# Optimization experiments

Measured on AMD Instinct MI355X. Metric: run time of the kernel, lower is better.

The kernel has to match this reference:

```python
import jax, jax.numpy as jnp
import numpy as np
import math

H_DIM = 1024
N_HEADS = 16
B, T = 2, 2048


def setup_inputs() -> dict:
    key = jax.random.key(0)
    ks = jax.random.split(key, 9)
    scale = 1.0 / math.sqrt(H_DIM)
    x = jax.random.normal(ks[0], (B, T, H_DIM), dtype=jnp.float32)
    Wq = jax.random.normal(ks[1], (H_DIM, H_DIM), dtype=jnp.float32) * scale
    Wk = jax.random.normal(ks[2], (H_DIM, H_DIM), dtype=jnp.float32) * scale
    Wv = jax.random.normal(ks[3], (H_DIM, H_DIM), dtype=jnp.float32) * scale
    Wp = jax.random.normal(ks[4], (H_DIM, H_DIM), dtype=jnp.float32) * scale
    bq = jnp.zeros((H_DIM,), dtype=jnp.float32)
    bk = jnp.zeros((H_DIM,), dtype=jnp.float32)
    bv = jnp.zeros((H_DIM,), dtype=jnp.float32)
    bp = jnp.zeros((H_DIM,), dtype=jnp.float32)
    return {"x": x, "Wq": Wq, "bq": bq, "Wk": Wk, "bk": bk,
            "Wv": Wv, "bv": bv, "Wp": Wp, "bp": bp}


def _attention(x, Wq, bq, Wk, bk, Wv, bv, Wp, bp):
    Bx, Tx, C = x.shape
    N = N_HEADS
    D = C // N
    # torch Linear: x @ W.T + b
    q = (x @ Wq.T + bq).reshape(Bx, Tx, N, D).transpose(0, 2, 1, 3)  # [B,N,T,D]
    k = (x @ Wk.T + bk).reshape(Bx, Tx, N, D).transpose(0, 2, 1, 3)
    v = (x @ Wv.T + bv).reshape(Bx, Tx, N, D).transpose(0, 2, 1, 3)
    scores = jnp.einsum('bntd,bnsd->bnts', q, k) / math.sqrt(D)  # [B,N,T,T]
    causal = jnp.tril(jnp.ones((Tx, Tx), dtype=bool))
    scores = jnp.where(causal[None, None], scores, -jnp.inf)
    probs = jax.nn.softmax(scores, axis=-1)
    attn = jnp.einsum('bnts,bnsd->bntd', probs, v)  # [B,N,T,D]
    attn = attn.transpose(0, 2, 1, 3).reshape(Bx, Tx, C)
    return attn @ Wp.T + bp


def reference(x, Wq, bq, Wk, bk, Wv, bv, Wp, bp):
    return _attention(x, Wq, bq, Wk, bk, Wv, bv, Wp, bp)
```

## Files before the change

### kernel.cpp

```cpp
#include <hip/hip_runtime.h>
#include <hip/hip_bf16.h>
#include <math.h>

#define TSEQ 2048
#define CDIM 1024
#define NHEADS 16
#define DHEAD 64
#define BSZ 2
#define MROWS (BSZ * TSEQ)
#define SCALE_Q 0.18033688f

typedef __attribute__((ext_vector_type(8))) short short8;
typedef __attribute__((ext_vector_type(4))) short short4v;
typedef __attribute__((ext_vector_type(4))) float f32x4;

__device__ inline f32x4 mfma16(short8 a, short8 b, f32x4 c) {
    return __builtin_amdgcn_mfma_f32_16x16x32_bf16(a, b, c, 0, 0, 0);
}

__device__ inline short f2bf(float f) {
    __hip_bfloat16 h = __float2bfloat16(f);
    return __builtin_bit_cast(short, h);
}

__global__ __launch_bounds__(256) void convx_kernel(const float* __restrict__ x,
                                                    short* __restrict__ xb) {
    size_t off = (size_t)(blockIdx.x * 256 + threadIdx.x) * 8;
    float4 a = *(const float4*)(x + off);
    float4 b = *(const float4*)(x + off + 4);
    short8 h;
    h[0] = f2bf(a.x); h[1] = f2bf(a.y); h[2] = f2bf(a.z); h[3] = f2bf(a.w);
    h[4] = f2bf(b.x); h[5] = f2bf(b.y); h[6] = f2bf(b.z); h[7] = f2bf(b.w);
    *(short8*)(xb + off) = h;
}

__global__ __launch_bounds__(256, 3) void gemm_qkv(
    const short* __restrict__ xb, const float* __restrict__ Wq,
    const float* __restrict__ Wk, const float* __restrict__ Wv,
    const float* __restrict__ bq, const float* __restrict__ bk,
    const float* __restrict__ bv, short* __restrict__ qws,
    short* __restrict__ kws, short* __restrict__ vtws) {
    __shared__ __attribute__((aligned(16))) short a_lds[128][72];
    __shared__ __attribute__((aligned(16))) short b_lds[128][72];

    const int tid = threadIdx.x;
    const int lane = tid & 63;
    const int wv = tid >> 6;
    const int wr = wv >> 1, wc = wv & 1;
    const int l15 = lane & 15, l4 = lane >> 4;
    const int mbase = blockIdx.x * 128;
    const int which = blockIdx.y >> 3;
    const int nbase = (blockIdx.y & 7) * 128;
    const float* Wf = which == 0 ? Wq : (which == 1 ? Wk : Wv);
    const float* bias = which == 0 ? bq : (which == 1 ? bk : bv);

    f32x4 acc[4][4];
#pragma unroll
    for (int i = 0; i < 4; ++i)
#pragma unroll
        for (int j = 0; j < 4; ++j) acc[i][j] = f32x4{0.f, 0.f, 0.f, 0.f};

    const int ar = tid >> 3;
    const int ag = (tid & 7) * 8;
    const int br = tid >> 4;
    const int bg = (tid & 15) * 4;
    const short* aptr = xb + (size_t)(mbase + ar) * CDIM + ag;
    const float* bptr = Wf + (size_t)(nbase + br) * CDIM + bg;

    short8 apre[4];
    float4 bpre[8];
#pragma unroll
    for (int it = 0; it < 4; ++it)
        apre[it] = *(const short8*)(aptr + (size_t)(32 * it) * CDIM);
#pragma unroll
    for (int it = 0; it < 8; ++it)
        bpre[it] = *(const float4*)(bptr + (size_t)(16 * it) * CDIM);

    for (int k0 = 0; k0 < CDIM; k0 += 64) {
        __syncthreads();
#pragma unroll
        for (int it = 0; it < 4; ++it)
            *(short8*)&a_lds[ar + 32 * it][ag] = apre[it];
#pragma unroll
        for (int it = 0; it < 8; ++it) {
            short4v h;
            h.x = f2bf(bpre[it].x); h.y = f2bf(bpre[it].y);
            h.z = f2bf(bpre[it].z); h.w = f2bf(bpre[it].w);
            *(short4v*)&b_lds[br + 16 * it][bg] = h;
        }
        __syncthreads();
        if (k0 + 64 < CDIM) {
#pragma unroll
            for (int it = 0; it < 4; ++it)
                apre[it] = *(const short8*)(aptr + (size_t)(32 * it) * CDIM + k0 + 64);
#pragma unroll
            for (int it = 0; it < 8; ++it)
                bpre[it] = *(const float4*)(bptr + (size_t)(16 * it) * CDIM + k0 + 64);
        }

#pragma unroll
        for (int kk = 0; kk < 2; ++kk) {
            short8 af[4], bfr[4];
#pragma unroll
            for (int i = 0; i < 4; ++i)
                af[i] = *(const short8*)&a_lds[wr * 64 + i * 16 + l15][kk * 32 + l4 * 8];
#pragma unroll
            for (int j = 0; j < 4; ++j)
                bfr[j] = *(const short8*)&b_lds[wc * 64 + j * 16 + l15][kk * 32 + l4 * 8];
#pragma unroll
            for (int i = 0; i < 4; ++i)
#pragma unroll
                for (int j = 0; j < 4; ++j)
                    acc[i][j] = mfma16(af[i], bfr[j], acc[i][j]);
        }
    }

    if (which < 2) {
        short* dst = which == 0 ? qws : kws;
        const float scale = which == 0 ? SCALE_Q : 1.0f;
#pragma unroll
        for (int i = 0; i < 4; ++i) {
            int mrow = mbase + wr * 64 + i * 16 + l4 * 4;
#pragma unroll
            for (int j = 0; j < 4; ++j) {
                int o = nbase + wc * 64 + j * 16 + l15;
                int n = o >> 6, d = o & 63;
                float bval = bias[o];
#pragma unroll
                for (int r = 0; r < 4; ++r) {
                    int mm = mrow + r;
                    int bb = mm >> 11;
                    int t = mm & (TSEQ - 1);
                    dst[(((size_t)bb * NHEADS + n) * TSEQ + t) * DHEAD + d] =
                        f2bf((acc[i][j][r] + bval) * scale);
                }
            }
        }
    } else {
#pragma unroll
        for (int i = 0; i < 4; ++i) {
            int mrow = mbase + wr * 64 + i * 16 + l4 * 4;
            int bb = mrow >> 11;
            int t = mrow & (TSEQ - 1);
#pragma unroll
            for (int j = 0; j < 4; ++j) {
                int o = nbase + wc * 64 + j * 16 + l15;
                int n = o >> 6, d = o & 63;
                float bval = bias[o];
                short4v h4;
#pragma unroll
                for (int r = 0; r < 4; ++r) h4[r] = f2bf(acc[i][j][r] + bval);
                *(short4v*)&vtws[(((size_t)bb * NHEADS + n) * DHEAD + d) * TSEQ + t] = h4;
            }
        }
    }
}

__global__ __launch_bounds__(256) void gemm_p(
    const short* __restrict__ attn, const short* __restrict__ wpb,
    const float* __restrict__ bp, float* __restrict__ out) {
    __shared__ __attribute__((aligned(16))) short a_lds[64][40];
    __shared__ __attribute__((aligned(16))) short b_lds[128][40];

    const int tid = threadIdx.x;
    const int lane = tid & 63;
    const int wv = tid >> 6;
    const int wr = wv >> 1, wc = wv & 1;
    const int l15 = lane & 15, l4 = lane >> 4;
    const int mbase = blockIdx.x * 64;
    const int nbase = blockIdx.y * 128;

    f32x4 acc[2][4];
#pragma unroll
    for (int i = 0; i < 2; ++i)
#pragma unroll
        for (int j = 0; j < 4; ++j) acc[i][j] = f32x4{0.f, 0.f, 0.f, 0.f};

    const int arow = tid >> 2;
    const int acol = (tid & 3) * 8;
    const short* aptr = attn + (size_t)(mbase + arow) * CDIM + acol;
    const short* bptr = wpb + (size_t)(nbase + arow) * CDIM + acol;

    short8 apre, bpre[2];
    apre = *(const short8*)(aptr);
    bpre[0] = *(const short8*)(bptr);
    bpre[1] = *(const short8*)(bptr + (size_t)64 * CDIM);

    for (int k0 = 0; k0 < CDIM; k0 += 32) {
        __syncthreads();
        *(short8*)&a_lds[arow][acol] = apre;
        *(short8*)&b_lds[arow][acol] = bpre[0];
        *(short8*)&b_lds[arow + 64][acol] = bpre[1];
        __syncthreads();
        if (k0 + 32 < CDIM) {
            apre = *(const short8*)(aptr + k0 + 32);
            bpre[0] = *(const short8*)(bptr + k0 + 32);
            bpre[1] = *(const short8*)(bptr + (size_t)64 * CDIM + k0 + 32);
        }

        short8 af[2], bfr[4];
#pragma unroll
        for (int i = 0; i < 2; ++i)
            af[i] = *(const short8*)&a_lds[wr * 32 + i * 16 + l15][l4 * 8];
#pragma unroll
        for (int j = 0; j < 4; ++j)
            bfr[j] = *(const short8*)&b_lds[wc * 64 + j * 16 + l15][l4 * 8];
#pragma unroll
        for (int i = 0; i < 2; ++i)
#pragma unroll
            for (int j = 0; j < 4; ++j)
                acc[i][j] = mfma16(af[i], bfr[j], acc[i][j]);
    }

#pragma unroll
    for (int i = 0; i < 2; ++i) {
        int mrow = mbase + wr * 32 + i * 16 + l4 * 4;
#pragma unroll
        for (int j = 0; j < 4; ++j) {
            int o = nbase + wc * 64 + j * 16 + l15;
            float bval = bp[o];
#pragma unroll
            for (int r = 0; r < 4; ++r)
                out[(size_t)(mrow + r) * CDIM + o] = acc[i][j][r] + bval;
        }
    }
}

__global__ __launch_bounds__(256) void attn_kernel(
    const short* __restrict__ q, const short* __restrict__ k,
    const short* __restrict__ vt, short* __restrict__ attn_out) {
    __shared__ __attribute__((aligned(16))) short k_lds[128][64];
    __shared__ __attribute__((aligned(16))) short vt_lds[64][128];
    __shared__ __attribute__((aligned(16))) short p_lds[4][16][136];

    const int tid = threadIdx.x;
    const int w = tid >> 6;
    const int lane = tid & 63;
    const int l15 = lane & 15;
    const int l4 = lane >> 4;
    const int h = blockIdx.x;
    const int qtile = gridDim.y - 1 - blockIdx.y;
    const int wrow0 = qtile * 64 + w * 16;

    short8 qf[2];
#pragma unroll
    for (int kh = 0; kh < 2; ++kh)
        qf[kh] = *(const short8*)(q + ((size_t)h * TSEQ + wrow0 + l15) * DHEAD +
                                  kh * 32 + l4 * 8);

    float l_run[4];
    f32x4 o_acc[4];
#pragma unroll
    for (int r = 0; r < 4; ++r) l_run[r] = 0.f;
#pragma unroll
    for (int dt = 0; dt < 4; ++dt) o_acc[dt] = f32x4{0.f, 0.f, 0.f, 0.f};

    const int ntiles = (qtile + 2) >> 1;
    const size_t kbase = (size_t)h * TSEQ * DHEAD;
    const size_t vbase = (size_t)h * DHEAD * TSEQ;

    const int ksrow = tid >> 3, ksg = tid & 7;
    const int vsrow = tid >> 4, vsg = tid & 15;

    short8 kpre[4], vpre[4];
#pragma unroll
    for (int it = 0; it < 4; ++it) {
        kpre[it] = *(const short8*)(k + kbase + (size_t)(ksrow + it * 32) * DHEAD + ksg * 8);
        vpre[it] = *(const short8*)(vt + vbase + (size_t)(vsrow + it * 16) * TSEQ + vsg * 8);
    }

    for (int kvt = 0; kvt < ntiles; ++kvt) {
        const int kvbase = kvt * 128;
        __syncthreads();
#pragma unroll
        for (int it = 0; it < 4; ++it) {
            int krow = ksrow + it * 32;
            *(short8*)&k_lds[krow][(ksg ^ (krow & 7)) * 8] = kpre[it];
            int vrow = vsrow + it * 16;
            *(short8*)&vt_lds[vrow][((vsg ^ (vrow & 15))) * 8] = vpre[it];
        }
        __syncthreads();
        if (kvt + 1 < ntiles) {
            int kvb2 = kvbase + 128;
#pragma unroll
            for (int it = 0; it < 4; ++it) {
                kpre[it] = *(const short8*)(k + kbase + (size_t)(kvb2 + ksrow + it * 32) * DHEAD + ksg * 8);
                vpre[it] = *(const short8*)(vt + vbase + (size_t)(vsrow + it * 16) * TSEQ + kvb2 + vsg * 8);
            }
        }

        f32x4 s[8];
#pragma unroll
        for (int jt = 0; jt < 8; ++jt) {
            int row = jt * 16 + l15;
            int sw = row & 7;
            short8 kf0 = *(const short8*)&k_lds[row][(l4 ^ sw) * 8];
            short8 kf1 = *(const short8*)&k_lds[row][((4 + l4) ^ sw) * 8];
            f32x4 a = f32x4{0.f, 0.f, 0.f, 0.f};
            a = mfma16(qf[0], kf0, a);
            a = mfma16(qf[1], kf1, a);
            s[jt] = a;
        }

        const bool needmask = (kvbase + 127 > wrow0);
#pragma unroll
        for (int r = 0; r < 4; ++r) {
            int qrow = wrow0 + l4 * 4 + r;
            float lp = 0.f;
#pragma unroll
            for (int jt = 0; jt < 8; ++jt) {
                float x = s[jt][r];
                if (needmask && (kvbase + jt * 16 + l15 > qrow)) x = -INFINITY;
                float e = __builtin_amdgcn_exp2f(x);
                lp += e;
                p_lds[w][l4 * 4 + r][jt * 16 + l15] = f2bf(e);
            }
            l_run[r] += lp;
        }

        short8 pa[4];
#pragma unroll
        for (int ks = 0; ks < 4; ++ks)
            pa[ks] = *(const short8*)&p_lds[w][l15][ks * 32 + l4 * 8];
#pragma unroll
        for (int dt = 0; dt < 4; ++dt) {
            int row = dt * 16 + l15;
            int sw = row & 15;
#pragma unroll
            for (int ks = 0; ks < 4; ++ks) {
                short8 vf = *(const short8*)&vt_lds[row][((ks * 4 + l4) ^ sw) * 8];
                o_acc[dt] = mfma16(pa[ks], vf, o_acc[dt]);
            }
        }
    }

#pragma unroll
    for (int r = 0; r < 4; ++r) {
        float l = l_run[r];
#pragma unroll
        for (int mk = 1; mk < 16; mk <<= 1) l += __shfl_xor(l, mk);
        l_run[r] = 1.0f / l;
    }
    const int b = h >> 4, n = h & 15;
#pragma unroll
    for (int dt = 0; dt < 4; ++dt) {
#pragma unroll
        for (int r = 0; r < 4; ++r) {
            int t = wrow0 + l4 * 4 + r;
            attn_out[((size_t)b * TSEQ + t) * CDIM + n * DHEAD + dt * 16 + l15] =
                f2bf(o_acc[dt][r] * l_run[r]);
        }
    }
}

extern "C" void kernel_launch(void* const* d_in, const int* in_sizes, int n_in,
                              void* d_out, int out_size, void* d_ws, size_t ws_size,
                              hipStream_t stream) {
    const float* x  = (const float*)d_in[0];
    const float* Wq = (const float*)d_in[1];
    const float* bq = (const float*)d_in[2];
    const float* Wk = (const float*)d_in[3];
    const float* bk = (const float*)d_in[4];
    const float* Wv = (const float*)d_in[5];
    const float* bv = (const float*)d_in[6];
    const float* Wp = (const float*)d_in[7];
    const float* bp = (const float*)d_in[8];

    char* ws = (char*)d_ws;
    const size_t SZ = (size_t)MROWS * CDIM * sizeof(short);
    short* qws  = (short*)(ws);
    short* kws  = (short*)(ws + SZ);
    short* vtws = (short*)(ws + 2 * SZ);
    short* xb   = (short*)(ws + 3 * SZ);
    short* attn = xb;
    short* wpb  = qws;

    convx_kernel<<<2048, 256, 0, stream>>>(x, xb);
    gemm_qkv<<<dim3(MROWS / 128, 24), 256, 0, stream>>>(xb, Wq, Wk, Wv, bq, bk, bv,
                                                         qws, kws, vtws);
    attn_kernel<<<dim3(BSZ * NHEADS, TSEQ / 64), 256, 0, stream>>>(qws, kws, vtws, attn);
    convx_kernel<<<512, 256, 0, stream>>>(Wp, wpb);
    gemm_p<<<dim3(MROWS / 64, CDIM / 128), 256, 0, stream>>>(attn, wpb, bp, (float*)d_out);
}
```

Before: 112.9 us.

## Pre-convert QKV weights to bf16 and stream GEMM tiles via global_load_lds

```diff
diff --git a/kernel.cpp b/kernel.cpp
--- a/kernel.cpp
+++ b/kernel.cpp
@@ -21,6 +21,12 @@
 __device__ inline short f2bf(float f) {
     __hip_bfloat16 h = __float2bfloat16(f);
     return __builtin_bit_cast(short, h);
+}
+
+__device__ inline void gl_lds16(const short* g, short* l) {
+    __builtin_amdgcn_global_load_lds(
+        (const __attribute__((address_space(1))) void*)g,
+        (__attribute__((address_space(3))) void*)l, 16, 0, 0);
 }
 
 __global__ __launch_bounds__(256) void convx_kernel(const float* __restrict__ x,
@@ -32,6 +38,126 @@
     h[0] = f2bf(a.x); h[1] = f2bf(a.y); h[2] = f2bf(a.z); h[3] = f2bf(a.w);
     h[4] = f2bf(b.x); h[5] = f2bf(b.y); h[6] = f2bf(b.z); h[7] = f2bf(b.w);
     *(short8*)(xb + off) = h;
+}
+
+__global__ __launch_bounds__(256) void conv3_kernel(
+    const float* __restrict__ swq, const float* __restrict__ swk,
+    const float* __restrict__ swv, short* __restrict__ wqb,
+    short* __restrict__ wkb, short* __restrict__ wvb) {
+    int chunk = blockIdx.x >> 9;
+    size_t off = (size_t)((blockIdx.x & 511) * 256 + threadIdx.x) * 8;
+    const float* s = chunk == 0 ? swq : (chunk == 1 ? swk : swv);
+    short* d = chunk == 0 ? wqb : (chunk == 1 ? wkb : wvb);
+    float4 a = *(const float4*)(s + off);
+    float4 b = *(const float4*)(s + off + 4);
+    short8 h;
+    h[0] = f2bf(a.x); h[1] = f2bf(a.y); h[2] = f2bf(a.z); h[3] = f2bf(a.w);
+    h[4] = f2bf(b.x); h[5] = f2bf(b.y); h[6] = f2bf(b.z); h[7] = f2bf(b.w);
+    *(short8*)(d + off) = h;
+}
+
+__global__ __launch_bounds__(256, 3) void gemm_qkv_g(
+    const short* __restrict__ xb, const short* __restrict__ wqb,
+    const short* __restrict__ wkb, const short* __restrict__ wvb,
+    const float* __restrict__ bq, const float* __restrict__ bk,
+    const float* __restrict__ bv, short* __restrict__ qws,
+    short* __restrict__ kws, short* __restrict__ vtws) {
+    __shared__ __attribute__((aligned(16))) short a_lds[128 * 64];
+    __shared__ __attribute__((aligned(16))) short b_lds[128 * 64];
+
+    const int tid = threadIdx.x;
+    const int lane = tid & 63;
+    const int wv = tid >> 6;
+    const int wr = wv >> 1, wc = wv & 1;
+    const int l15 = lane & 15, l4 = lane >> 4;
+    const int mbase = blockIdx.x * 128;
+    const int which = blockIdx.y >> 3;
+    const int nbase = (blockIdx.y & 7) * 128;
+    const short* Wb = which == 0 ? wqb : (which == 1 ? wkb : wvb);
+    const float* bias = which == 0 ? bq : (which == 1 ? bk : bv);
+
+    f32x4 acc[4][4];
+#pragma unroll
+    for (int i = 0; i < 4; ++i)
+#pragma unroll
+        for (int j = 0; j < 4; ++j) acc[i][j] = f32x4{0.f, 0.f, 0.f, 0.f};
+
+    const int srow = tid >> 3;
+    const int gcol = (tid & 7) ^ (srow & 7);
+    const short* asrc = xb + (size_t)(mbase + srow) * CDIM + gcol * 8;
+    const short* bsrc = Wb + (size_t)(nbase + srow) * CDIM + gcol * 8;
+    short* adst = &a_lds[tid * 8];
+    short* bdst = &b_lds[tid * 8];
+
+    for (int k0 = 0; k0 < CDIM; k0 += 64) {
+        __syncthreads();
+#pragma unroll
+        for (int it = 0; it < 4; ++it) {
+            gl_lds16(asrc + (size_t)(it * 32) * CDIM + k0, adst + it * 2048);
+            gl_lds16(bsrc + (size_t)(it * 32) * CDIM + k0, bdst + it * 2048);
+        }
+        __syncthreads();
+
+#pragma unroll
+        for (int kk = 0; kk < 2; ++kk) {
+            short8 af[4], bfr[4];
+#pragma unroll
+            for (int i = 0; i < 4; ++i) {
+                int R = wr * 64 + i * 16 + l15;
+                af[i] = *(const short8*)&a_lds[R * 64 + ((kk * 4 + l4) ^ (R & 7)) * 8];
+            }
+#pragma unroll
+            for (int j = 0; j < 4; ++j) {
+                int R = wc * 64 + j * 16 + l15;
+                bfr[j] = *(const short8*)&b_lds[R * 64 + ((kk * 4 + l4) ^ (R & 7)) * 8];
+            }
+#pragma unroll
+            for (int i = 0; i < 4; ++i)
+#pragma unroll
+                for (int j = 0; j < 4; ++j)
+                    acc[i][j] = mfma16(af[i], bfr[j], acc[i][j]);
+        }
+    }
+
+    if (which < 2) {
+        short* dst = which == 0 ? qws : kws;
+        const float scale = which == 0 ? SCALE_Q : 1.0f;
+#pragma unroll
+        for (int i = 0; i < 4; ++i) {
+            int mrow = mbase + wr * 64 + i * 16 + l4 * 4;
+#pragma unroll
+            for (int j = 0; j < 4; ++j) {
+                int o = nbase + wc * 64 + j * 16 + l15;
+                int n = o >> 6, d = o & 63;
+                float bval = bias[o];
+#pragma unroll
+                for (int r = 0; r < 4; ++r) {
+                    int mm = mrow + r;
+                    int bb = mm >> 11;
+                    int t = mm & (TSEQ - 1);
+                    dst[(((size_t)bb * NHEADS + n) * TSEQ + t) * DHEAD + d] =
+                        f2bf((acc[i][j][r] + bval) * scale);
+                }
+            }
+        }
+    } else {
+#pragma unroll
+        for (int i = 0; i < 4; ++i) {
+            int mrow = mbase + wr * 64 + i * 16 + l4 * 4;
+            int bb = mrow >> 11;
+            int t = mrow & (TSEQ - 1);
+#pragma unroll
+            for (int j = 0; j < 4; ++j) {
+                int o = nbase + wc * 64 + j * 16 + l15;
+                int n = o >> 6, d = o & 63;
+                float bval = bias[o];
+                short4v h4;
+#pragma unroll
+                for (int r = 0; r < 4; ++r) h4[r] = f2bf(acc[i][j][r] + bval);
+                *(short4v*)&vtws[(((size_t)bb * NHEADS + n) * DHEAD + d) * TSEQ + t] = h4;
+            }
+        }
+    }
 }
 
 __global__ __launch_bounds__(256, 3) void gemm_qkv(
@@ -376,8 +502,20 @@
     short* wpb  = qws;
 
     convx_kernel<<<2048, 256, 0, stream>>>(x, xb);
-    gemm_qkv<<<dim3(MROWS / 128, 24), 256, 0, stream>>>(xb, Wq, Wk, Wv, bq, bk, bv,
-                                                         qws, kws, vtws);
+
+    const size_t WSZ = (size_t)CDIM * CDIM * sizeof(short);
+    if (ws_size >= 4 * SZ + 3 * WSZ) {
+        short* wqb = (short*)(ws + 4 * SZ);
+        short* wkb = wqb + (size_t)CDIM * CDIM;
+        short* wvb = wkb + (size_t)CDIM * CDIM;
+        conv3_kernel<<<1536, 256, 0, stream>>>(Wq, Wk, Wv, wqb, wkb, wvb);
+        gemm_qkv_g<<<dim3(MROWS / 128, 24), 256, 0, stream>>>(
+            xb, wqb, wkb, wvb, bq, bk, bv, qws, kws, vtws);
+    } else {
+        gemm_qkv<<<dim3(MROWS / 128, 24), 256, 0, stream>>>(
+            xb, Wq, Wk, Wv, bq, bk, bv, qws, kws, vtws);
+    }
+
     attn_kernel<<<dim3(BSZ * NHEADS, TSEQ / 64), 256, 0, stream>>>(qws, kws, vtws, attn);
     convx_kernel<<<512, 256, 0, stream>>>(Wp, wpb);
     gemm_p<<<dim3(MROWS / 64, CDIM / 128), 256, 0, stream>>>(attn, wpb, bp, (float*)d_out);
```

Result: no change. 112.7 us (-0.2%).
